# Kernel tuning notes

Hardware: AMD Instinct MI355X
Metric: run time of the kernel (lower is better)

## Reference

```python
import jax, jax.numpy as jnp
import numpy as np
import math

C = 256
K = 64
STAGE_NUM = 3
UNFOLD_SIZES = (1, 3, 5)


def _l2norm(t, axis):
    return t / (1e-6 + jnp.linalg.norm(t, axis=axis, keepdims=True))


def setup_inputs() -> dict:
    key = jax.random.key(0)
    k0, k1, k2 = jax.random.split(key, 3)
    b, h, w = 4, 64, 64
    x = jax.random.normal(k0, (b, C, h, w), dtype=jnp.float32)
    mu0 = jax.random.normal(k1, (1, C, K), dtype=jnp.float32) * math.sqrt(2.0 / K)
    mu0 = _l2norm(mu0, axis=1)  # matches buffer init: normal_(0, sqrt(2/k)) then l2norm over c
    w_scalar = jnp.array(1.0, dtype=jnp.float32)
    # convcat: Conv2d(3c, c, 1); init std = sqrt(2 / (1*1*out_channels)) = sqrt(2/c)
    w_cat = jax.random.normal(k2, (C, 3 * C), dtype=jnp.float32) * math.sqrt(2.0 / C)
    b_cat = jnp.zeros((C,), dtype=jnp.float32)
    return {"x": x, "mu0": mu0, "w": w_scalar, "w_cat": w_cat, "b_cat": b_cat}


def _mwi_forward(x, mu0, w, w_cat, b_cat):
    b, c, h, wd = x.shape
    k = mu0.shape[2]
    mu = jnp.broadcast_to(mu0, (b, c, k))
    feats = []
    for s in UNFOLD_SIZES:
        p = (s - 1) // 2
        xp = jnp.pad(x, ((0, 0), (0, 0), (p, p), (p, p)))
        # im2col: (b, c, s*s, h, w), kernel positions row-major -> matches torch F.unfold then view(b,c,-1)
        patches = jnp.stack([xp[:, :, i:i + h, j:j + wd] for i in range(s) for j in range(s)], axis=2)
        ux = patches.reshape(b, c, s * s * h * wd)  # (b, c, N)
        z = None
        for _ in range(STAGE_NUM):  # EM iterations (no_grad in original)
            z = jax.nn.softmax(jnp.einsum('bcn,bck->bnk', ux, mu), axis=2)  # E-step
            z_ = z / (1e-6 + z.sum(axis=1, keepdims=True))
            mu = _l2norm(jnp.einsum('bcn,bnk->bck', ux, z_), axis=1)  # M-step
        mu = jax.lax.stop_gradient(mu)
        z = jax.lax.stop_gradient(z)
        zf = jnp.einsum('bck,bnk->bcn', mu, z)  # reconstruction (b, c, N)
        zf = zf.reshape(b, c, s, s, h, wd)
        # col2im (F.fold): overlap-add of kernel positions
        out = jnp.zeros((b, c, h + 2 * p, wd + 2 * p), dtype=x.dtype)
        for i in range(s):
            for j in range(s):
                out = out.at[:, :, i:i + h, j:j + wd].add(zf[:, :, i, j])
        feats.append(out[:, :, p:p + h, p:p + wd])
    cat = jnp.concatenate(feats, axis=1)  # (b, 3c, h, w)
    u = jnp.einsum('bihw,oi->bohw', cat, w_cat) + b_cat[None, :, None, None]
    out = jax.nn.relu(u * w + x)
    return out, mu


def reference(x, mu0, w, w_cat, b_cat):
    return _mwi_forward(x, mu0, w, w_cat, b_cat)
```

## Files before the change

kernel.cpp:

```cpp
#include <hip/hip_runtime.h>

typedef float f32x4 __attribute__((ext_vector_type(4)));
typedef short bf16x8 __attribute__((ext_vector_type(8)));
typedef unsigned short u16;
typedef u16 u16x8 __attribute__((ext_vector_type(8)));
typedef unsigned int u32;

#define B 4
#define C 256
#define K 64
#define NN 4096
#define W3C 768
#define CP 264
#define SP 72
#define LGP 68

__device__ __forceinline__ u16 bf_hi(float f) {
    unsigned u = __float_as_uint(f);
    u += 0x7FFFu + ((u >> 16) & 1u);
    return (u16)(u >> 16);
}
__device__ __forceinline__ float bf_f(u16 s) { return __uint_as_float(((unsigned)s) << 16); }

__global__ void k_prep(const float* __restrict__ x, const float* __restrict__ mu0,
                       const float* __restrict__ w_cat,
                       u16* __restrict__ xch, u16* __restrict__ xcl,
                       u16* __restrict__ wch, u16* __restrict__ wcl,
                       u16* __restrict__ muth, u16* __restrict__ mutl,
                       float* __restrict__ tp0) {
    int blk = blockIdx.x, tid = threadIdx.x;
    if (blk < 2048) {
        int i = blk * 256 + tid;
        const float4* s4 = (const float4*)(x + (size_t)i * 8);
        float4 a = s4[0], bq = s4[1];
        float v[8] = {a.x, a.y, a.z, a.w, bq.x, bq.y, bq.z, bq.w};
        u16x8 hv, lv;
        #pragma unroll
        for (int j = 0; j < 8; j++) { u16 hh = bf_hi(v[j]); hv[j] = hh; lv[j] = bf_hi(v[j] - bf_f(hh)); }
        *(u16x8*)(xch + (size_t)i * 8) = hv;
        *(u16x8*)(xcl + (size_t)i * 8) = lv;
    } else if (blk < 2144) {
        int i = (blk - 2048) * 256 + tid;
        const float4* s4 = (const float4*)(w_cat + (size_t)i * 8);
        float4 a = s4[0], bq = s4[1];
        float v[8] = {a.x, a.y, a.z, a.w, bq.x, bq.y, bq.z, bq.w};
        u16x8 hv, lv;
        #pragma unroll
        for (int j = 0; j < 8; j++) { u16 hh = bf_hi(v[j]); hv[j] = hh; lv[j] = bf_hi(v[j] - bf_f(hh)); }
        *(u16x8*)(wch + (size_t)i * 8) = hv;
        *(u16x8*)(wcl + (size_t)i * 8) = lv;
    } else if (blk < 2400) {
        int g = (blk - 2144) * 256 + tid;
        int kq = (g >> 8) & 63, cq = g & 255;
        float v = mu0[cq * K + kq];
        u16 hh = bf_hi(v);
        muth[g] = hh;
        mutl[g] = bf_hi(v - bf_f(hh));
    } else {
        int i = (blk - 2400) * 256 + tid;
        float4 z = {0.f, 0.f, 0.f, 0.f};
        *(float4*)&tp0[(size_t)i * 4] = z;
    }
}

__global__ void k_prept(const float* __restrict__ x, u16* __restrict__ th,
                        u16* __restrict__ tl) {
    __shared__ float tile[32][33];
    int b = blockIdx.z, c0 = blockIdx.y * 32, n0 = blockIdx.x * 32;
    int tx = threadIdx.x, ty = threadIdx.y;
    #pragma unroll
    for (int j = 0; j < 4; j++)
        tile[ty + j * 8][tx] = x[((size_t)(b * C + c0 + ty + j * 8)) * NN + n0 + tx];
    __syncthreads();
    #pragma unroll
    for (int j = 0; j < 4; j++) {
        int n = n0 + ty + j * 8;
        float v = tile[tx][ty + j * 8];
        u16 hh = bf_hi(v);
        size_t o = ((size_t)(b * NN + n)) * C + c0 + tx;
        th[o] = hh;
        tl[o] = bf_hi(v - bf_f(hh));
    }
}

__global__ __launch_bounds__(512) void k_em(
        const u16* __restrict__ xth, const u16* __restrict__ xtl,
        const u16* __restrict__ xch, const u16* __restrict__ xcl,
        const u16* __restrict__ muth, const u16* __restrict__ mutl,
        const float* __restrict__ tp_prev, float* __restrict__ tp_cur,
        float* __restrict__ tp_next, float* __restrict__ dpart,
        u16* __restrict__ sig_out, u16* __restrict__ Pb,
        const u16* __restrict__ wch, const u16* __restrict__ wcl,
        int iter, int pv, float dconst_prev, int write_sig, int s_prev)
{
    extern __shared__ char smem[];
    u16* smh   = (u16*)smem;
    u16* sml   = smh + 64 * CP;
    float* slog = (float*)(sml + 64 * CP);
    u16* sTh   = (u16*)(slog + 64 * LGP);
    u16* sTl   = sTh + 64 * SP;
    float* redf = (float*)(sTl + 64 * SP);

    const int ch = blockIdx.x, b = blockIdx.y, tid = threadIdx.x;
    const int n0 = ch * 64;
    const int w = tid >> 6, l = tid & 63, lg = l >> 4, lr = l & 15;
    f32x4 z4 = {0.f, 0.f, 0.f, 0.f};

    if (tid < 256) tp_next[(size_t)b * K * C + ch * 256 + tid] = 0.f;

    float vals[32];
    float inv = 0.f;
    int kq = tid >> 3, g = tid & 7;
    if (iter == 0) {
        size_t mbase = (size_t)(b * K) * C;
        for (int t = tid; t < 2048; t += 512) {
            int r = t >> 5, cof = (t & 31) * 8;
            *(u16x8*)&smh[r * CP + cof] = *(const u16x8*)&muth[mbase + (size_t)r * C + cof];
            *(u16x8*)&sml[r * CP + cof] = *(const u16x8*)&mutl[mbase + (size_t)r * C + cof];
        }
    } else {
        if (tid < 64) {
            float dv = 0.f;
            #pragma unroll 8
            for (int c2 = 0; c2 < 64; c2++) dv += dpart[((size_t)(b * 64 + c2)) * K + tid];
            redf[1088 + tid] = dv;
        }
        const float* tp = tp_prev + (size_t)b * K * C + (size_t)kq * C + g * 32;
        float ssq = 0.f;
        #pragma unroll
        for (int j4 = 0; j4 < 8; j4++) {
            float4 v4 = *(const float4*)&tp[j4 * 4];
            vals[j4 * 4 + 0] = v4.x; vals[j4 * 4 + 1] = v4.y;
            vals[j4 * 4 + 2] = v4.z; vals[j4 * 4 + 3] = v4.w;
            ssq += v4.x * v4.x + v4.y * v4.y + v4.z * v4.z + v4.w * v4.w;
        }
        #pragma unroll
        for (int off = 1; off <= 4; off <<= 1) ssq += __shfl_xor(ssq, off);
        __syncthreads();
        float d = dconst_prev + redf[1088 + kq];
        inv = 1.f / (1e-6f * d + sqrtf(ssq));
        #pragma unroll
        for (int j8 = 0; j8 < 4; j8++) {
            u16x8 hv, lv;
            #pragma unroll
            for (int j = 0; j < 8; j++) {
                float v = vals[j8 * 8 + j] * inv;
                u16 hh = bf_hi(v);
                hv[j] = hh; lv[j] = bf_hi(v - bf_f(hh));
            }
            *(u16x8*)&smh[kq * CP + g * 32 + j8 * 8] = hv;
            *(u16x8*)&sml[kq * CP + g * 32 + j8 * 8] = lv;
        }
    }
    __syncthreads();

    if (s_prev >= 0 && ch < 4) {
        f32x4 pacc[2] = {z4, z4};
        int orow = ch * 64 + (w & 3) * 16 + lr;
        const u16* wbh = wch + (size_t)orow * W3C + s_prev * C;
        const u16* wbl = wcl + (size_t)orow * W3C + s_prev * C;
        for (int cc = 0; cc < 8; cc++) {
            int co = cc * 32 + lg * 8;
            bf16x8 Ah = *(const bf16x8*)&wbh[co];
            bf16x8 Al = *(const bf16x8*)&wbl[co];
            #pragma unroll
            for (int ktl = 0; ktl < 2; ktl++) {
                int kt = (w >> 2) * 2 + ktl;
                bf16x8 Bh = *(bf16x8*)&smh[(kt * 16 + lr) * CP + co];
                bf16x8 Bl = *(bf16x8*)&sml[(kt * 16 + lr) * CP + co];
                pacc[ktl] = __builtin_amdgcn_mfma_f32_16x16x32_bf16(Ah, Bh, pacc[ktl], 0, 0, 0);
                pacc[ktl] = __builtin_amdgcn_mfma_f32_16x16x32_bf16(Al, Bh, pacc[ktl], 0, 0, 0);
                pacc[ktl] = __builtin_amdgcn_mfma_f32_16x16x32_bf16(Ah, Bl, pacc[ktl], 0, 0, 0);
            }
        }
        #pragma unroll
        for (int ktl = 0; ktl < 2; ktl++)
            #pragma unroll
            for (int jj = 0; jj < 4; jj++) {
                int o = ch * 64 + (w & 3) * 16 + lg * 4 + jj;
                int kk = ((w >> 2) * 2 + ktl) * 16 + lr;
                Pb[((size_t)((s_prev * B + b) * C + o)) * K + kk] = bf_hi(pacc[ktl][jj]);
            }
    }

    f32x4 acc[4] = {z4, z4, z4, z4};
    {
        int chalf = (w >> 2) * 128;
        const u16* xrh = xth + ((size_t)(b * NN + n0 + (w & 3) * 16 + lr)) * C + chalf;
        const u16* xrl = xtl + ((size_t)(b * NN + n0 + (w & 3) * 16 + lr)) * C + chalf;
        for (int cc = 0; cc < 4; cc++) {
            int co = cc * 32 + lg * 8;
            bf16x8 Ah = *(const bf16x8*)&xrh[co];
            bf16x8 Al = *(const bf16x8*)&xrl[co];
            #pragma unroll
            for (int kt = 0; kt < 4; kt++) {
                bf16x8 Bh = *(bf16x8*)&smh[(kt * 16 + lr) * CP + chalf + co];
                bf16x8 Bl = *(bf16x8*)&sml[(kt * 16 + lr) * CP + chalf + co];
                acc[kt] = __builtin_amdgcn_mfma_f32_16x16x32_bf16(Ah, Bh, acc[kt], 0, 0, 0);
                acc[kt] = __builtin_amdgcn_mfma_f32_16x16x32_bf16(Al, Bh, acc[kt], 0, 0, 0);
                acc[kt] = __builtin_amdgcn_mfma_f32_16x16x32_bf16(Ah, Bl, acc[kt], 0, 0, 0);
            }
        }
    }
    if (w < 4) {
        #pragma unroll
        for (int kt = 0; kt < 4; kt++)
            #pragma unroll
            for (int jj = 0; jj < 4; jj++)
                slog[((w & 3) * 16 + lg * 4 + jj) * LGP + kt * 16 + lr] = acc[kt][jj];
    }
    __syncthreads();

    if (w >= 4) {
        float swv[4][4];
        float psum[4] = {0.f, 0.f, 0.f, 0.f};
        #pragma unroll
        for (int jj = 0; jj < 4; jj++) {
            int rloc = (w & 3) * 16 + lg * 4 + jj;
            int n = n0 + rloc;
            float v0 = acc[0][jj] + slog[rloc * LGP + 0 * 16 + lr];
            float v1 = acc[1][jj] + slog[rloc * LGP + 1 * 16 + lr];
            float v2 = acc[2][jj] + slog[rloc * LGP + 2 * 16 + lr];
            float v3 = acc[3][jj] + slog[rloc * LGP + 3 * 16 + lr];
            float m = fmaxf(fmaxf(v0, v1), fmaxf(v2, v3));
            #pragma unroll
            for (int off = 1; off <= 8; off <<= 1) m = fmaxf(m, __shfl_xor(m, off));
            float e0 = __expf(v0 - m), e1 = __expf(v1 - m), e2 = __expf(v2 - m), e3 = __expf(v3 - m);
            float ss = e0 + e1 + e2 + e3;
            #pragma unroll
            for (int off = 1; off <= 8; off <<= 1) ss += __shfl_xor(ss, off);
            int y = n >> 6, xx = n & 63;
            float cnt = (float)((min(pv, y) + min(pv, 63 - y) + 1) * (min(pv, xx) + min(pv, 63 - xx) + 1));
            float sc = cnt / ss;
            swv[jj][0] = e0 * sc; swv[jj][1] = e1 * sc; swv[jj][2] = e2 * sc; swv[jj][3] = e3 * sc;
            #pragma unroll
            for (int kt = 0; kt < 4; kt++) {
                psum[kt] += swv[jj][kt];
                if (write_sig)
                    sig_out[((size_t)(b * NN + n)) * K + kt * 16 + lr] = bf_hi(swv[jj][kt]);
            }
        }
        #pragma unroll
        for (int kt = 0; kt < 4; kt++) {
            #pragma unroll
            for (int jp = 0; jp < 2; jp++) {
                float va = swv[2 * jp][kt], vb = swv[2 * jp + 1][kt];
                u16 ha = bf_hi(va), hb = bf_hi(vb);
                u16 la = bf_hi(va - bf_f(ha)), lb = bf_hi(vb - bf_f(hb));
                int col = (w & 3) * 16 + lg * 4 + 2 * jp;
                *(u32*)&sTh[(kt * 16 + lr) * SP + col] = (u32)ha | ((u32)hb << 16);
                *(u32*)&sTl[(kt * 16 + lr) * SP + col] = (u32)la | ((u32)lb << 16);
            }
            redf[(kt * 16 + lr) * 17 + (w & 3) * 4 + lg] = psum[kt];
        }
    }
    __syncthreads();
    if (tid < 64) {
        float sd = 0.f;
        #pragma unroll
        for (int g2 = 0; g2 < 16; g2++) sd += redf[tid * 17 + g2];
        dpart[((size_t)(b * 64 + ch)) * K + tid] = sd;
    }

    f32x4 macc[8];
    #pragma unroll
    for (int t = 0; t < 8; t++) macc[t] = z4;
    #pragma unroll
    for (int nn2 = 0; nn2 < 2; nn2++) {
        int no = nn2 * 32 + lg * 8;
        bf16x8 Ah[4], Al[4];
        #pragma unroll
        for (int kt2 = 0; kt2 < 4; kt2++) {
            Ah[kt2] = *(bf16x8*)&sTh[(kt2 * 16 + lr) * SP + no];
            Al[kt2] = *(bf16x8*)&sTl[(kt2 * 16 + lr) * SP + no];
        }
        #pragma unroll
        for (int cio = 0; cio < 2; cio++) {
            int c = (w * 2 + cio) * 16 + lr;
            size_t go = ((size_t)(b * C + c)) * NN + n0 + no;
            bf16x8 Bh = *(const bf16x8*)&xch[go];
            bf16x8 Bl = *(const bf16x8*)&xcl[go];
            #pragma unroll
            for (int kt2 = 0; kt2 < 4; kt2++) {
                macc[kt2 * 2 + cio] = __builtin_amdgcn_mfma_f32_16x16x32_bf16(Ah[kt2], Bh, macc[kt2 * 2 + cio], 0, 0, 0);
                macc[kt2 * 2 + cio] = __builtin_amdgcn_mfma_f32_16x16x32_bf16(Al[kt2], Bh, macc[kt2 * 2 + cio], 0, 0, 0);
                macc[kt2 * 2 + cio] = __builtin_amdgcn_mfma_f32_16x16x32_bf16(Ah[kt2], Bl, macc[kt2 * 2 + cio], 0, 0, 0);
            }
        }
    }
    #pragma unroll
    for (int kt2 = 0; kt2 < 4; kt2++)
        #pragma unroll
        for (int cio = 0; cio < 2; cio++)
            #pragma unroll
            for (int jj = 0; jj < 4; jj++) {
                int kk = kt2 * 16 + lg * 4 + jj;
                int c = (w * 2 + cio) * 16 + lr;
                atomicAdd(&tp_cur[((size_t)b * K + kk) * C + c], macc[kt2 * 2 + cio][jj]);
            }
}

__global__ __launch_bounds__(256) void k_pfinal(
        const float* __restrict__ tp_last, const float* __restrict__ dpart,
        const u16* __restrict__ wch, const u16* __restrict__ wcl,
        u16* __restrict__ Pb, float* __restrict__ out_mu, float dconst)
{
    extern __shared__ char smem[];
    u16* smh = (u16*)smem;
    u16* sml = smh + 64 * CP;
    float* redf = (float*)(sml + 64 * CP);
    int ob = blockIdx.x, b = blockIdx.y, tid = threadIdx.x;
    int w = tid >> 6, l = tid & 63, lg = l >> 4, lr = l & 15;
    if (tid < 64) {
        float dv = 0.f;
        #pragma unroll 8
        for (int c2 = 0; c2 < 64; c2++) dv += dpart[((size_t)(b * 64 + c2)) * K + tid];
        redf[tid] = dv;
    }
    __syncthreads();
    {
        int kq = tid >> 2, g = tid & 3;
        const float* tp = tp_last + (size_t)b * K * C + (size_t)kq * C + g * 64;
        float vals[64];
        float ssq = 0.f;
        #pragma unroll
        for (int j4 = 0; j4 < 16; j4++) {
            float4 v4 = *(const float4*)&tp[j4 * 4];
            vals[j4 * 4 + 0] = v4.x; vals[j4 * 4 + 1] = v4.y;
            vals[j4 * 4 + 2] = v4.z; vals[j4 * 4 + 3] = v4.w;
            ssq += v4.x * v4.x + v4.y * v4.y + v4.z * v4.z + v4.w * v4.w;
        }
        ssq += __shfl_xor(ssq, 1);
        ssq += __shfl_xor(ssq, 2);
        float d = dconst + redf[kq];
        float inv = 1.f / (1e-6f * d + sqrtf(ssq));
        #pragma unroll
        for (int j8 = 0; j8 < 8; j8++) {
            u16x8 hv, lv;
            #pragma unroll
            for (int j = 0; j < 8; j++) {
                float v = vals[j8 * 8 + j] * inv;
                u16 hh = bf_hi(v);
                hv[j] = hh; lv[j] = bf_hi(v - bf_f(hh));
            }
            *(u16x8*)&smh[kq * CP + g * 64 + j8 * 8] = hv;
            *(u16x8*)&sml[kq * CP + g * 64 + j8 * 8] = lv;
        }
        if (ob == 0) {
            #pragma unroll 8
            for (int j = 0; j < 64; j++)
                out_mu[((size_t)(b * C + g * 64 + j)) * K + kq] = vals[j] * inv;
        }
    }
    __syncthreads();
    f32x4 pacc[4] = {{0.f,0.f,0.f,0.f},{0.f,0.f,0.f,0.f},{0.f,0.f,0.f,0.f},{0.f,0.f,0.f,0.f}};
    int orow = ob * 64 + w * 16 + lr;
    const u16* wbh = wch + (size_t)orow * W3C + 2 * C;
    const u16* wbl = wcl + (size_t)orow * W3C + 2 * C;
    for (int cc = 0; cc < 8; cc++) {
        int co = cc * 32 + lg * 8;
        bf16x8 Ah = *(const bf16x8*)&wbh[co];
        bf16x8 Al = *(const bf16x8*)&wbl[co];
        #pragma unroll
        for (int kt = 0; kt < 4; kt++) {
            bf16x8 Bh = *(bf16x8*)&smh[(kt * 16 + lr) * CP + co];
            bf16x8 Bl = *(bf16x8*)&sml[(kt * 16 + lr) * CP + co];
            pacc[kt] = __builtin_amdgcn_mfma_f32_16x16x32_bf16(Ah, Bh, pacc[kt], 0, 0, 0);
            pacc[kt] = __builtin_amdgcn_mfma_f32_16x16x32_bf16(Al, Bh, pacc[kt], 0, 0, 0);
            pacc[kt] = __builtin_amdgcn_mfma_f32_16x16x32_bf16(Ah, Bl, pacc[kt], 0, 0, 0);
        }
    }
    #pragma unroll
    for (int kt = 0; kt < 4; kt++)
        #pragma unroll
        for (int jj = 0; jj < 4; jj++) {
            int o = ob * 64 + w * 16 + lg * 4 + jj;
            Pb[((size_t)((2 * B + b) * C + o)) * K + kt * 16 + lr] = bf_hi(pacc[kt][jj]);
        }
}

__global__ __launch_bounds__(256) void k_final(
        const u16* __restrict__ sh_g, const u16* __restrict__ Pb,
        const float* __restrict__ x, const float* __restrict__ b_cat,
        const float* __restrict__ wscal, float* __restrict__ out) {
    __shared__ u16 ssig[64 * 72];
    __shared__ u16 sP[64 * 72];
    __shared__ float tbuf[64 * 68];
    int nt = blockIdx.x, ot = blockIdx.y, b = blockIdx.z;
    int n0 = nt * 64, o0 = ot * 64;
    int tid = threadIdx.x, w = tid >> 6, l = tid & 63, lg = l >> 4, lr = l & 15;
    f32x4 z4 = {0.f, 0.f, 0.f, 0.f};
    f32x4 acc[4] = {z4, z4, z4, z4};
    for (int s = 0; s < 3; s++) {
        __syncthreads();
        for (int t = tid; t < 512; t += 256) {
            int r = t >> 3, kc = (t & 7) * 8;
            *(u16x8*)&ssig[r * 72 + kc] =
                *(const u16x8*)&sh_g[(size_t)s * ((size_t)B * NN * K) + ((size_t)(b * NN + n0 + r)) * K + kc];
            *(u16x8*)&sP[r * 72 + kc] =
                *(const u16x8*)&Pb[((size_t)((s * B + b) * C + o0 + r)) * K + kc];
        }
        __syncthreads();
        #pragma unroll
        for (int kk = 0; kk < 2; kk++) {
            int ko = kk * 32 + lg * 8;
            bf16x8 A = *(bf16x8*)&ssig[(w * 16 + lr) * 72 + ko];
            #pragma unroll
            for (int oi = 0; oi < 4; oi++) {
                bf16x8 Bv = *(bf16x8*)&sP[(oi * 16 + lr) * 72 + ko];
                acc[oi] = __builtin_amdgcn_mfma_f32_16x16x32_bf16(A, Bv, acc[oi], 0, 0, 0);
            }
        }
    }
    __syncthreads();
    #pragma unroll
    for (int oi = 0; oi < 4; oi++)
        #pragma unroll
        for (int jj = 0; jj < 4; jj++)
            tbuf[(oi * 16 + lr) * 68 + (w * 16 + lg * 4 + jj)] = acc[oi][jj];
    __syncthreads();
    float wv = wscal[0];
    for (int t = tid; t < 1024; t += 256) {
        int ol = t >> 4, ck = (t & 15) * 4;
        int o = o0 + ol;
        float bc = b_cat[o];
        float4 u4 = *(float4*)&tbuf[ol * 68 + ck];
        size_t base = ((size_t)(b * C + o)) * NN + n0 + ck;
        float4 xv = *(const float4*)&x[base];
        float4 r;
        r.x = fmaxf((u4.x + bc) * wv + xv.x, 0.f);
        r.y = fmaxf((u4.y + bc) * wv + xv.y, 0.f);
        r.z = fmaxf((u4.z + bc) * wv + xv.z, 0.f);
        r.w = fmaxf((u4.w + bc) * wv + xv.w, 0.f);
        *(float4*)&out[base] = r;
    }
}

extern "C" void kernel_launch(void* const* d_in, const int* in_sizes, int n_in,
                              void* d_out, int out_size, void* d_ws, size_t ws_size,
                              hipStream_t stream) {
    const float* x     = (const float*)d_in[0];
    const float* mu0   = (const float*)d_in[1];
    const float* wsc   = (const float*)d_in[2];
    const float* w_cat = (const float*)d_in[3];
    const float* b_cat = (const float*)d_in[4];
    float* out = (float*)d_out;
    char* wsb = (char*)d_ws;

    const size_t SZ_X2   = (size_t)B * C * NN * 2;
    const size_t SZ_MUT  = (size_t)B * K * C * 2;
    const size_t SZ_SIGH = (size_t)3 * B * NN * K * 2;
    const size_t SZ_TPB  = (size_t)B * K * C * 4;
    const size_t SZ_DP   = (size_t)B * 64 * K * 4;
    const size_t SZ_PB   = (size_t)3 * B * C * K * 2;
    const size_t SZ_WC   = (size_t)C * W3C * 2;

    size_t off = 0;
    u16*   xch  = (u16*)(wsb + off); off += SZ_X2;
    u16*   xcl  = (u16*)(wsb + off); off += SZ_X2;
    u16*   xth  = (u16*)(wsb + off); off += SZ_X2;
    u16*   xtl  = (u16*)(wsb + off); off += SZ_X2;
    u16*   muth = (u16*)(wsb + off); off += SZ_MUT;
    u16*   mutl = (u16*)(wsb + off); off += SZ_MUT;
    u16*   sigh = (u16*)(wsb + off); off += SZ_SIGH;
    float* tpb0 = (float*)(wsb + off); off += SZ_TPB;
    float* tpb1 = (float*)(wsb + off); off += SZ_TPB;
    float* tpb2 = (float*)(wsb + off); off += SZ_TPB;
    float* dpart= (float*)(wsb + off); off += SZ_DP;
    u16*   Pb   = (u16*)(wsb + off); off += SZ_PB;
    u16*   wch  = (u16*)(wsb + off); off += SZ_WC;
    u16*   wcl  = (u16*)(wsb + off); off += SZ_WC;
    float* out_mu = out + (size_t)B * C * NN;
    float* bufs[3] = {tpb0, tpb1, tpb2};

    const int EM_LDS = 2 * 64 * CP * 2 + 64 * LGP * 4 + 2 * 64 * SP * 2 + 1152 * 4;
    const int PF_LDS = 2 * 64 * CP * 2 + 64 * 4;
    hipFuncSetAttribute((const void*)k_em, hipFuncAttributeMaxDynamicSharedMemorySize, EM_LDS);
    hipFuncSetAttribute((const void*)k_pfinal, hipFuncAttributeMaxDynamicSharedMemorySize, PF_LDS);

    k_prep<<<2464, 256, 0, stream>>>(x, mu0, w_cat, xch, xcl, wch, wcl, muth, mutl, tpb0);
    k_prept<<<dim3(128, 8, B), dim3(32, 8), 0, stream>>>(x, xth, xtl);

    const int   pvals[3]   = {0, 1, 2};
    const float dconsts[3] = {1e-6f, 1e-6f + 11.9375f, 1e-6f + 59.4375f};

    for (int i = 0; i < 9; i++) {
        int s = i / 3;
        u16* shs = sigh + (size_t)s * ((size_t)B * NN * K);
        float dprev = (i > 0) ? dconsts[(i - 1) / 3] : 0.f;
        int s_prev = (i > 0 && i % 3 == 0) ? (i / 3 - 1) : -1;
        k_em<<<dim3(64, B), 512, EM_LDS, stream>>>(
            xth, xtl, xch, xcl, muth, mutl,
            bufs[(i + 2) % 3], bufs[i % 3], bufs[(i + 1) % 3], dpart,
            shs, Pb, wch, wcl,
            i, pvals[s], dprev, (i % 3 == 2) ? 1 : 0, s_prev);
    }
    k_pfinal<<<dim3(4, B), 256, PF_LDS, stream>>>(bufs[8 % 3], dpart, wch, wcl,
                                                  Pb, out_mu, dconsts[2]);
    k_final<<<dim3(64, 4, B), 256, 0, stream>>>(sigh, Pb, x, b_cat, wsc, out);
}
```

Measured before the change: 290.7 us.

## Fuse prep, EM iterations and pfinal into one persistent kernel with grid barriers

```diff
diff --git a/kernel.cpp b/kernel.cpp
--- a/kernel.cpp
+++ b/kernel.cpp
@@ -22,123 +22,144 @@
 }
 __device__ __forceinline__ float bf_f(u16 s) { return __uint_as_float(((unsigned)s) << 16); }
 
-__global__ void k_prep(const float* __restrict__ x, const float* __restrict__ mu0,
-                       const float* __restrict__ w_cat,
-                       u16* __restrict__ xch, u16* __restrict__ xcl,
-                       u16* __restrict__ wch, u16* __restrict__ wcl,
-                       u16* __restrict__ muth, u16* __restrict__ mutl,
-                       float* __restrict__ tp0) {
-    int blk = blockIdx.x, tid = threadIdx.x;
-    if (blk < 2048) {
-        int i = blk * 256 + tid;
-        const float4* s4 = (const float4*)(x + (size_t)i * 8);
-        float4 a = s4[0], bq = s4[1];
-        float v[8] = {a.x, a.y, a.z, a.w, bq.x, bq.y, bq.z, bq.w};
-        u16x8 hv, lv;
-        #pragma unroll
-        for (int j = 0; j < 8; j++) { u16 hh = bf_hi(v[j]); hv[j] = hh; lv[j] = bf_hi(v[j] - bf_f(hh)); }
-        *(u16x8*)(xch + (size_t)i * 8) = hv;
-        *(u16x8*)(xcl + (size_t)i * 8) = lv;
-    } else if (blk < 2144) {
-        int i = (blk - 2048) * 256 + tid;
-        const float4* s4 = (const float4*)(w_cat + (size_t)i * 8);
-        float4 a = s4[0], bq = s4[1];
-        float v[8] = {a.x, a.y, a.z, a.w, bq.x, bq.y, bq.z, bq.w};
-        u16x8 hv, lv;
-        #pragma unroll
-        for (int j = 0; j < 8; j++) { u16 hh = bf_hi(v[j]); hv[j] = hh; lv[j] = bf_hi(v[j] - bf_f(hh)); }
-        *(u16x8*)(wch + (size_t)i * 8) = hv;
-        *(u16x8*)(wcl + (size_t)i * 8) = lv;
-    } else if (blk < 2400) {
-        int g = (blk - 2144) * 256 + tid;
-        int kq = (g >> 8) & 63, cq = g & 255;
-        float v = mu0[cq * K + kq];
-        u16 hh = bf_hi(v);
-        muth[g] = hh;
-        mutl[g] = bf_hi(v - bf_f(hh));
-    } else {
-        int i = (blk - 2400) * 256 + tid;
-        float4 z = {0.f, 0.f, 0.f, 0.f};
-        *(float4*)&tp0[(size_t)i * 4] = z;
-    }
+__device__ __forceinline__ void gridbar(u32* cnt, u32 target) {
+    __syncthreads();
+    if (threadIdx.x == 0) {
+        __threadfence();
+        __hip_atomic_fetch_add(cnt, 1u, __ATOMIC_ACQ_REL, __HIP_MEMORY_SCOPE_AGENT);
+        while (__hip_atomic_load(cnt, __ATOMIC_ACQUIRE, __HIP_MEMORY_SCOPE_AGENT) < target)
+            __builtin_amdgcn_s_sleep(2);
+        __threadfence();
+    }
+    __syncthreads();
 }
 
-__global__ void k_prept(const float* __restrict__ x, u16* __restrict__ th,
-                        u16* __restrict__ tl) {
-    __shared__ float tile[32][33];
-    int b = blockIdx.z, c0 = blockIdx.y * 32, n0 = blockIdx.x * 32;
-    int tx = threadIdx.x, ty = threadIdx.y;
-    #pragma unroll
-    for (int j = 0; j < 4; j++)
-        tile[ty + j * 8][tx] = x[((size_t)(b * C + c0 + ty + j * 8)) * NN + n0 + tx];
-    __syncthreads();
-    #pragma unroll
-    for (int j = 0; j < 4; j++) {
-        int n = n0 + ty + j * 8;
-        float v = tile[tx][ty + j * 8];
-        u16 hh = bf_hi(v);
-        size_t o = ((size_t)(b * NN + n)) * C + c0 + tx;
-        th[o] = hh;
-        tl[o] = bf_hi(v - bf_f(hh));
-    }
-}
-
-__global__ __launch_bounds__(512) void k_em(
-        const u16* __restrict__ xth, const u16* __restrict__ xtl,
-        const u16* __restrict__ xch, const u16* __restrict__ xcl,
-        const u16* __restrict__ muth, const u16* __restrict__ mutl,
-        const float* __restrict__ tp_prev, float* __restrict__ tp_cur,
-        float* __restrict__ tp_next, float* __restrict__ dpart,
-        u16* __restrict__ sig_out, u16* __restrict__ Pb,
-        const u16* __restrict__ wch, const u16* __restrict__ wcl,
-        int iter, int pv, float dconst_prev, int write_sig, int s_prev)
+__global__ __launch_bounds__(512, 2) void k_mwi(
+        const float* __restrict__ x, const float* __restrict__ mu0,
+        const float* __restrict__ w_cat,
+        u16* __restrict__ xch, u16* __restrict__ xcl,
+        u16* __restrict__ xth, u16* __restrict__ xtl,
+        u16* __restrict__ sigh,
+        float* __restrict__ tp0, float* __restrict__ tp1, float* __restrict__ tp2,
+        float* __restrict__ dpart, u16* __restrict__ Pb,
+        u16* __restrict__ wch, u16* __restrict__ wcl,
+        float* __restrict__ out_mu, u32* __restrict__ cnt)
 {
     extern __shared__ char smem[];
-    u16* smh   = (u16*)smem;
-    u16* sml   = smh + 64 * CP;
+    u16* smh = (u16*)smem;
+    u16* sml = smh + 64 * CP;
     float* slog = (float*)(sml + 64 * CP);
-    u16* sTh   = (u16*)(slog + 64 * LGP);
-    u16* sTl   = sTh + 64 * SP;
+    u16* sTh = (u16*)(slog + 64 * LGP);
+    u16* sTl = sTh + 64 * SP;
     float* redf = (float*)(sTl + 64 * SP);
+    float* tpose = (float*)smem;
 
     const int ch = blockIdx.x, b = blockIdx.y, tid = threadIdx.x;
+    const int blk = b * 64 + ch;
     const int n0 = ch * 64;
+
+    for (int r = 0; r < 8; r++) {
+        int t = blk * 16 + r * 2 + (tid >> 8);
+        int b2 = t >> 10, rem = t & 1023;
+        int c0 = (rem >> 7) << 5, m0 = (rem & 127) << 5;
+        float* tb = tpose + (tid >> 8) * 1056;
+        int tx = tid & 31, ty = (tid >> 5) & 7;
+        #pragma unroll
+        for (int j = 0; j < 4; j++)
+            tb[(ty + j * 8) * 33 + tx] = x[((size_t)(b2 * C + c0 + ty + j * 8)) * NN + m0 + tx];
+        __syncthreads();
+        #pragma unroll
+        for (int j = 0; j < 4; j++) {
+            float v = tb[tx * 33 + ty + j * 8];
+            u16 hh = bf_hi(v);
+            size_t o = ((size_t)(b2 * NN + m0 + ty + j * 8)) * C + c0 + tx;
+            xth[o] = hh;
+            xtl[o] = bf_hi(v - bf_f(hh));
+        }
+        __syncthreads();
+    }
+    {
+        int gtid = blk * 512 + tid;
+        for (int idx = gtid; idx < 524288 + 24576; idx += 131072) {
+            const float* s8; u16 *dh, *dl; size_t o8;
+            if (idx < 524288) { s8 = x + (size_t)idx * 8; dh = xch; dl = xcl; o8 = (size_t)idx * 8; }
+            else { int j2 = idx - 524288; s8 = w_cat + (size_t)j2 * 8; dh = wch; dl = wcl; o8 = (size_t)j2 * 8; }
+            float4 a = ((const float4*)s8)[0], bq = ((const float4*)s8)[1];
+            float v[8] = {a.x, a.y, a.z, a.w, bq.x, bq.y, bq.z, bq.w};
+            u16x8 hv, lv;
+            #pragma unroll
+            for (int j = 0; j < 8; j++) { u16 hh = bf_hi(v[j]); hv[j] = hh; lv[j] = bf_hi(v[j] - bf_f(hh)); }
+            *(u16x8*)(dh + o8) = hv;
+            *(u16x8*)(dl + o8) = lv;
+        }
+        if (gtid < 65536) tp0[gtid] = 0.f;
+    }
+    gridbar(cnt, 256);
+
     const int w = tid >> 6, l = tid & 63, lg = l >> 4, lr = l & 15;
+    const int chalf = (w >> 2) * 128;
+    bf16x8 eAh[4], eAl[4];
+    {
+        const u16* xrh = xth + ((size_t)(b * NN + n0 + (w & 3) * 16 + lr)) * C + chalf;
+        const u16* xrl = xtl + ((size_t)(b * NN + n0 + (w & 3) * 16 + lr)) * C + chalf;
+        #pragma unroll
+        for (int cc = 0; cc < 4; cc++) {
+            eAh[cc] = *(const bf16x8*)&xrh[cc * 32 + lg * 8];
+            eAl[cc] = *(const bf16x8*)&xrl[cc * 32 + lg * 8];
+        }
+    }
+    bf16x8 mBh[4], mBl[4];
+    #pragma unroll
+    for (int nn2 = 0; nn2 < 2; nn2++)
+        #pragma unroll
+        for (int cio = 0; cio < 2; cio++) {
+            int c = (w * 2 + cio) * 16 + lr;
+            size_t go = ((size_t)(b * C + c)) * NN + n0 + nn2 * 32 + lg * 8;
+            mBh[nn2 * 2 + cio] = *(const bf16x8*)&xch[go];
+            mBl[nn2 * 2 + cio] = *(const bf16x8*)&xcl[go];
+        }
+
     f32x4 z4 = {0.f, 0.f, 0.f, 0.f};
-
-    if (tid < 256) tp_next[(size_t)b * K * C + ch * 256 + tid] = 0.f;
-
-    float vals[32];
-    float inv = 0.f;
-    int kq = tid >> 3, g = tid & 7;
-    if (iter == 0) {
-        size_t mbase = (size_t)(b * K) * C;
-        for (int t = tid; t < 2048; t += 512) {
-            int r = t >> 5, cof = (t & 31) * 8;
-            *(u16x8*)&smh[r * CP + cof] = *(const u16x8*)&muth[mbase + (size_t)r * C + cof];
-            *(u16x8*)&sml[r * CP + cof] = *(const u16x8*)&mutl[mbase + (size_t)r * C + cof];
-        }
-    } else {
-        if (tid < 64) {
-            float dv = 0.f;
-            #pragma unroll 8
-            for (int c2 = 0; c2 < 64; c2++) dv += dpart[((size_t)(b * 64 + c2)) * K + tid];
-            redf[1088 + tid] = dv;
-        }
-        const float* tp = tp_prev + (size_t)b * K * C + (size_t)kq * C + g * 32;
-        float ssq = 0.f;
-        #pragma unroll
-        for (int j4 = 0; j4 < 8; j4++) {
-            float4 v4 = *(const float4*)&tp[j4 * 4];
-            vals[j4 * 4 + 0] = v4.x; vals[j4 * 4 + 1] = v4.y;
-            vals[j4 * 4 + 2] = v4.z; vals[j4 * 4 + 3] = v4.w;
-            ssq += v4.x * v4.x + v4.y * v4.y + v4.z * v4.z + v4.w * v4.w;
-        }
-        #pragma unroll
-        for (int off = 1; off <= 4; off <<= 1) ssq += __shfl_xor(ssq, off);
-        __syncthreads();
-        float d = dconst_prev + redf[1088 + kq];
-        inv = 1.f / (1e-6f * d + sqrtf(ssq));
+    const int kq = tid >> 3, g = tid & 7;
+
+    for (int i = 0; i <= 9; i++) {
+        const bool last = (i == 9);
+        if (last && ch >= 4) return;
+        int ip = i % 3, inx = (i + 1) % 3, ipv = (i + 2) % 3;
+        float* tp_cur  = ip  == 0 ? tp0 : (ip  == 1 ? tp1 : tp2);
+        float* tp_next = inx == 0 ? tp0 : (inx == 1 ? tp1 : tp2);
+        const float* tp_prev = ipv == 0 ? tp0 : (ipv == 1 ? tp1 : tp2);
+
+        float vals[32];
+        float inv;
+        if (i == 0) {
+            #pragma unroll
+            for (int j = 0; j < 32; j++) vals[j] = mu0[(g * 32 + j) * K + kq];
+            inv = 1.f;
+        } else {
+            if (tid < 64) {
+                float dv = 0.f;
+                #pragma unroll 8
+                for (int c2 = 0; c2 < 64; c2++) dv += dpart[((size_t)(b * 64 + c2)) * K + tid];
+                redf[1088 + tid] = dv;
+            }
+            const float* tp = tp_prev + (size_t)b * K * C + (size_t)kq * C + g * 32;
+            float ssq = 0.f;
+            #pragma unroll
+            for (int j4 = 0; j4 < 8; j4++) {
+                float4 v4 = *(const float4*)&tp[j4 * 4];
+                vals[j4 * 4 + 0] = v4.x; vals[j4 * 4 + 1] = v4.y;
+                vals[j4 * 4 + 2] = v4.z; vals[j4 * 4 + 3] = v4.w;
+                ssq += v4.x * v4.x + v4.y * v4.y + v4.z * v4.z + v4.w * v4.w;
+            }
+            #pragma unroll
+            for (int off = 1; off <= 4; off <<= 1) ssq += __shfl_xor(ssq, off);
+            __syncthreads();
+            int si = (i - 1) / 3;
+            float dc = 1e-6f + (si == 0 ? 0.f : (si == 1 ? 11.9375f : 59.4375f));
+            float d = dc + redf[1088 + kq];
+            inv = 1.f / (1e-6f * d + sqrtf(ssq));
+        }
         #pragma unroll
         for (int j8 = 0; j8 < 4; j8++) {
             u16x8 hv, lv;
@@ -151,232 +172,159 @@
             *(u16x8*)&smh[kq * CP + g * 32 + j8 * 8] = hv;
             *(u16x8*)&sml[kq * CP + g * 32 + j8 * 8] = lv;
         }
-    }
-    __syncthreads();
-
-    if (s_prev >= 0 && ch < 4) {
-        f32x4 pacc[2] = {z4, z4};
-        int orow = ch * 64 + (w & 3) * 16 + lr;
-        const u16* wbh = wch + (size_t)orow * W3C + s_prev * C;
-        const u16* wbl = wcl + (size_t)orow * W3C + s_prev * C;
-        for (int cc = 0; cc < 8; cc++) {
-            int co = cc * 32 + lg * 8;
-            bf16x8 Ah = *(const bf16x8*)&wbh[co];
-            bf16x8 Al = *(const bf16x8*)&wbl[co];
-            #pragma unroll
-            for (int ktl = 0; ktl < 2; ktl++) {
-                int kt = (w >> 2) * 2 + ktl;
+        __syncthreads();
+
+        int sp = (i > 0 && i % 3 == 0) ? (i / 3 - 1) : -1;
+        if (sp >= 0 && ch < 4) {
+            f32x4 pacc[2] = {z4, z4};
+            int orow = ch * 64 + (w & 3) * 16 + lr;
+            const u16* wbh = wch + (size_t)orow * W3C + sp * C;
+            const u16* wbl = wcl + (size_t)orow * W3C + sp * C;
+            for (int cc2 = 0; cc2 < 8; cc2++) {
+                int co = cc2 * 32 + lg * 8;
+                bf16x8 Ah = *(const bf16x8*)&wbh[co];
+                bf16x8 Al = *(const bf16x8*)&wbl[co];
+                #pragma unroll
+                for (int ktl = 0; ktl < 2; ktl++) {
+                    int kt = (w >> 2) * 2 + ktl;
+                    bf16x8 Bh = *(bf16x8*)&smh[(kt * 16 + lr) * CP + co];
+                    bf16x8 Bl = *(bf16x8*)&sml[(kt * 16 + lr) * CP + co];
+                    pacc[ktl] = __builtin_amdgcn_mfma_f32_16x16x32_bf16(Ah, Bh, pacc[ktl], 0, 0, 0);
+                    pacc[ktl] = __builtin_amdgcn_mfma_f32_16x16x32_bf16(Al, Bh, pacc[ktl], 0, 0, 0);
+                    pacc[ktl] = __builtin_amdgcn_mfma_f32_16x16x32_bf16(Ah, Bl, pacc[ktl], 0, 0, 0);
+                }
+            }
+            #pragma unroll
+            for (int ktl = 0; ktl < 2; ktl++)
+                #pragma unroll
+                for (int jj = 0; jj < 4; jj++) {
+                    int o = ch * 64 + (w & 3) * 16 + lg * 4 + jj;
+                    int kk = ((w >> 2) * 2 + ktl) * 16 + lr;
+                    Pb[((size_t)((sp * B + b) * C + o)) * K + kk] = bf_hi(pacc[ktl][jj]);
+                }
+        }
+        if (last) {
+            if (ch == 0) {
+                #pragma unroll
+                for (int j = 0; j < 32; j++)
+                    out_mu[((size_t)(b * C + g * 32 + j)) * K + kq] = vals[j] * inv;
+            }
+            return;
+        }
+
+        if (tid < 256) tp_next[(size_t)b * K * C + ch * 256 + tid] = 0.f;
+
+        f32x4 acc[4] = {z4, z4, z4, z4};
+        #pragma unroll
+        for (int cc = 0; cc < 4; cc++) {
+            int co = chalf + cc * 32 + lg * 8;
+            #pragma unroll
+            for (int kt = 0; kt < 4; kt++) {
                 bf16x8 Bh = *(bf16x8*)&smh[(kt * 16 + lr) * CP + co];
                 bf16x8 Bl = *(bf16x8*)&sml[(kt * 16 + lr) * CP + co];
-                pacc[ktl] = __builtin_amdgcn_mfma_f32_16x16x32_bf16(Ah, Bh, pacc[ktl], 0, 0, 0);
-                pacc[ktl] = __builtin_amdgcn_mfma_f32_16x16x32_bf16(Al, Bh, pacc[ktl], 0, 0, 0);
-                pacc[ktl] = __builtin_amdgcn_mfma_f32_16x16x32_bf16(Ah, Bl, pacc[ktl], 0, 0, 0);
-            }
-        }
-        #pragma unroll
-        for (int ktl = 0; ktl < 2; ktl++)
+                acc[kt] = __builtin_amdgcn_mfma_f32_16x16x32_bf16(eAh[cc], Bh, acc[kt], 0, 0, 0);
+                acc[kt] = __builtin_amdgcn_mfma_f32_16x16x32_bf16(eAl[cc], Bh, acc[kt], 0, 0, 0);
+                acc[kt] = __builtin_amdgcn_mfma_f32_16x16x32_bf16(eAh[cc], Bl, acc[kt], 0, 0, 0);
+            }
+        }
+        if (w < 4) {
+            #pragma unroll
+            for (int kt = 0; kt < 4; kt++)
+                #pragma unroll
+                for (int jj = 0; jj < 4; jj++)
+                    slog[((w & 3) * 16 + lg * 4 + jj) * LGP + kt * 16 + lr] = acc[kt][jj];
+        }
+        __syncthreads();
+
+        if (w >= 4) {
+            int pv = i / 3;
+            int write_sig = (i % 3 == 2);
+            u16* sig_out = sigh + (size_t)(i / 3) * ((size_t)B * NN * K);
+            float swv[4][4];
+            float psum[4] = {0.f, 0.f, 0.f, 0.f};
             #pragma unroll
             for (int jj = 0; jj < 4; jj++) {
-                int o = ch * 64 + (w & 3) * 16 + lg * 4 + jj;
-                int kk = ((w >> 2) * 2 + ktl) * 16 + lr;
-                Pb[((size_t)((s_prev * B + b) * C + o)) * K + kk] = bf_hi(pacc[ktl][jj]);
-            }
-    }
-
-    f32x4 acc[4] = {z4, z4, z4, z4};
-    {
-        int chalf = (w >> 2) * 128;
-        const u16* xrh = xth + ((size_t)(b * NN + n0 + (w & 3) * 16 + lr)) * C + chalf;
-        const u16* xrl = xtl + ((size_t)(b * NN + n0 + (w & 3) * 16 + lr)) * C + chalf;
-        for (int cc = 0; cc < 4; cc++) {
-            int co = cc * 32 + lg * 8;
-            bf16x8 Ah = *(const bf16x8*)&xrh[co];
-            bf16x8 Al = *(const bf16x8*)&xrl[co];
+                int rloc = (w & 3) * 16 + lg * 4 + jj;
+                int n = n0 + rloc;
+                float v0 = acc[0][jj] + slog[rloc * LGP + 0 * 16 + lr];
+                float v1 = acc[1][jj] + slog[rloc * LGP + 1 * 16 + lr];
+                float v2 = acc[2][jj] + slog[rloc * LGP + 2 * 16 + lr];
+                float v3 = acc[3][jj] + slog[rloc * LGP + 3 * 16 + lr];
+                float m = fmaxf(fmaxf(v0, v1), fmaxf(v2, v3));
+                #pragma unroll
+                for (int off = 1; off <= 8; off <<= 1) m = fmaxf(m, __shfl_xor(m, off));
+                float e0 = __expf(v0 - m), e1 = __expf(v1 - m), e2 = __expf(v2 - m), e3 = __expf(v3 - m);
+                float ss = e0 + e1 + e2 + e3;
+                #pragma unroll
+                for (int off = 1; off <= 8; off <<= 1) ss += __shfl_xor(ss, off);
+                int y = n >> 6, xx = n & 63;
+                float cntw = (float)((min(pv, y) + min(pv, 63 - y) + 1) * (min(pv, xx) + min(pv, 63 - xx) + 1));
+                float sc = cntw / ss;
+                swv[jj][0] = e0 * sc; swv[jj][1] = e1 * sc; swv[jj][2] = e2 * sc; swv[jj][3] = e3 * sc;
+                #pragma unroll
+                for (int kt = 0; kt < 4; kt++) {
+                    psum[kt] += swv[jj][kt];
+                    if (write_sig)
+                        sig_out[((size_t)(b * NN + n)) * K + kt * 16 + lr] = bf_hi(swv[jj][kt]);
+                }
+            }
             #pragma unroll
             for (int kt = 0; kt < 4; kt++) {
-                bf16x8 Bh = *(bf16x8*)&smh[(kt * 16 + lr) * CP + chalf + co];
-                bf16x8 Bl = *(bf16x8*)&sml[(kt * 16 + lr) * CP + chalf + co];
-                acc[kt] = __builtin_amdgcn_mfma_f32_16x16x32_bf16(Ah, Bh, acc[kt], 0, 0, 0);
-                acc[kt] = __builtin_amdgcn_mfma_f32_16x16x32_bf16(Al, Bh, acc[kt], 0, 0, 0);
-                acc[kt] = __builtin_amdgcn_mfma_f32_16x16x32_bf16(Ah, Bl, acc[kt], 0, 0, 0);
-            }
-        }
-    }
-    if (w < 4) {
-        #pragma unroll
-        for (int kt = 0; kt < 4; kt++)
-            #pragma unroll
-            for (int jj = 0; jj < 4; jj++)
-                slog[((w & 3) * 16 + lg * 4 + jj) * LGP + kt * 16 + lr] = acc[kt][jj];
-    }
-    __syncthreads();
-
-    if (w >= 4) {
-        float swv[4][4];
-        float psum[4] = {0.f, 0.f, 0.f, 0.f};
-        #pragma unroll
-        for (int jj = 0; jj < 4; jj++) {
-            int rloc = (w & 3) * 16 + lg * 4 + jj;
-            int n = n0 + rloc;
-            float v0 = acc[0][jj] + slog[rloc * LGP + 0 * 16 + lr];
-            float v1 = acc[1][jj] + slog[rloc * LGP + 1 * 16 + lr];
-            float v2 = acc[2][jj] + slog[rloc * LGP + 2 * 16 + lr];
-            float v3 = acc[3][jj] + slog[rloc * LGP + 3 * 16 + lr];
-            float m = fmaxf(fmaxf(v0, v1), fmaxf(v2, v3));
-            #pragma unroll
-            for (int off = 1; off <= 8; off <<= 1) m = fmaxf(m, __shfl_xor(m, off));
-            float e0 = __expf(v0 - m), e1 = __expf(v1 - m), e2 = __expf(v2 - m), e3 = __expf(v3 - m);
-            float ss = e0 + e1 + e2 + e3;
-            #pragma unroll
-            for (int off = 1; off <= 8; off <<= 1) ss += __shfl_xor(ss, off);
-            int y = n >> 6, xx = n & 63;
-            float cnt = (float)((min(pv, y) + min(pv, 63 - y) + 1) * (min(pv, xx) + min(pv, 63 - xx) + 1));
-            float sc = cnt / ss;
-            swv[jj][0] = e0 * sc; swv[jj][1] = e1 * sc; swv[jj][2] = e2 * sc; swv[jj][3] = e3 * sc;
-            #pragma unroll
-            for (int kt = 0; kt < 4; kt++) {
-                psum[kt] += swv[jj][kt];
-                if (write_sig)
-                    sig_out[((size_t)(b * NN + n)) * K + kt * 16 + lr] = bf_hi(swv[jj][kt]);
-            }
-        }
-        #pragma unroll
-        for (int kt = 0; kt < 4; kt++) {
-            #pragma unroll
-            for (int jp = 0; jp < 2; jp++) {
-                float va = swv[2 * jp][kt], vb = swv[2 * jp + 1][kt];
-                u16 ha = bf_hi(va), hb = bf_hi(vb);
-                u16 la = bf_hi(va - bf_f(ha)), lb = bf_hi(vb - bf_f(hb));
-                int col = (w & 3) * 16 + lg * 4 + 2 * jp;
-                *(u32*)&sTh[(kt * 16 + lr) * SP + col] = (u32)ha | ((u32)hb << 16);
-                *(u32*)&sTl[(kt * 16 + lr) * SP + col] = (u32)la | ((u32)lb << 16);
-            }
-            redf[(kt * 16 + lr) * 17 + (w & 3) * 4 + lg] = psum[kt];
-        }
-    }
-    __syncthreads();
-    if (tid < 64) {
-        float sd = 0.f;
-        #pragma unroll
-        for (int g2 = 0; g2 < 16; g2++) sd += redf[tid * 17 + g2];
-        dpart[((size_t)(b * 64 + ch)) * K + tid] = sd;
-    }
-
-    f32x4 macc[8];
-    #pragma unroll
-    for (int t = 0; t < 8; t++) macc[t] = z4;
-    #pragma unroll
-    for (int nn2 = 0; nn2 < 2; nn2++) {
-        int no = nn2 * 32 + lg * 8;
-        bf16x8 Ah[4], Al[4];
-        #pragma unroll
-        for (int kt2 = 0; kt2 < 4; kt2++) {
-            Ah[kt2] = *(bf16x8*)&sTh[(kt2 * 16 + lr) * SP + no];
-            Al[kt2] = *(bf16x8*)&sTl[(kt2 * 16 + lr) * SP + no];
-        }
-        #pragma unroll
-        for (int cio = 0; cio < 2; cio++) {
-            int c = (w * 2 + cio) * 16 + lr;
-            size_t go = ((size_t)(b * C + c)) * NN + n0 + no;
-            bf16x8 Bh = *(const bf16x8*)&xch[go];
-            bf16x8 Bl = *(const bf16x8*)&xcl[go];
+                #pragma unroll
+                for (int jp = 0; jp < 2; jp++) {
+                    float va = swv[2 * jp][kt], vb = swv[2 * jp + 1][kt];
+                    u16 ha = bf_hi(va), hb = bf_hi(vb);
+                    u16 la = bf_hi(va - bf_f(ha)), lb = bf_hi(vb - bf_f(hb));
+                    int col = (w & 3) * 16 + lg * 4 + 2 * jp;
+                    *(u32*)&sTh[(kt * 16 + lr) * SP + col] = (u32)ha | ((u32)hb << 16);
+                    *(u32*)&sTl[(kt * 16 + lr) * SP + col] = (u32)la | ((u32)lb << 16);
+                }
+                redf[(kt * 16 + lr) * 17 + (w & 3) * 4 + lg] = psum[kt];
+            }
+        }
+        __syncthreads();
+        if (tid < 64) {
+            float sd = 0.f;
+            #pragma unroll
+            for (int g2 = 0; g2 < 16; g2++) sd += redf[tid * 17 + g2];
+            dpart[((size_t)(b * 64 + ch)) * K + tid] = sd;
+        }
+
+        f32x4 macc[8];
+        #pragma unroll
+        for (int t2 = 0; t2 < 8; t2++) macc[t2] = z4;
+        #pragma unroll
+        for (int nn2 = 0; nn2 < 2; nn2++) {
+            int no = nn2 * 32 + lg * 8;
+            bf16x8 Ah[4], Al[4];
             #pragma unroll
             for (int kt2 = 0; kt2 < 4; kt2++) {
-                macc[kt2 * 2 + cio] = __builtin_amdgcn_mfma_f32_16x16x32_bf16(Ah[kt2], Bh, macc[kt2 * 2 + cio], 0, 0, 0);
-                macc[kt2 * 2 + cio] = __builtin_amdgcn_mfma_f32_16x16x32_bf16(Al[kt2], Bh, macc[kt2 * 2 + cio], 0, 0, 0);
-                macc[kt2 * 2 + cio] = __builtin_amdgcn_mfma_f32_16x16x32_bf16(Ah[kt2], Bl, macc[kt2 * 2 + cio], 0, 0, 0);
-            }
-        }
-    }
-    #pragma unroll
-    for (int kt2 = 0; kt2 < 4; kt2++)
-        #pragma unroll
-        for (int cio = 0; cio < 2; cio++)
-            #pragma unroll
-            for (int jj = 0; jj < 4; jj++) {
-                int kk = kt2 * 16 + lg * 4 + jj;
-                int c = (w * 2 + cio) * 16 + lr;
-                atomicAdd(&tp_cur[((size_t)b * K + kk) * C + c], macc[kt2 * 2 + cio][jj]);
-            }
-}
-
-__global__ __launch_bounds__(256) void k_pfinal(
-        const float* __restrict__ tp_last, const float* __restrict__ dpart,
-        const u16* __restrict__ wch, const u16* __restrict__ wcl,
-        u16* __restrict__ Pb, float* __restrict__ out_mu, float dconst)
-{
-    extern __shared__ char smem[];
-    u16* smh = (u16*)smem;
-    u16* sml = smh + 64 * CP;
-    float* redf = (float*)(sml + 64 * CP);
-    int ob = blockIdx.x, b = blockIdx.y, tid = threadIdx.x;
-    int w = tid >> 6, l = tid & 63, lg = l >> 4, lr = l & 15;
-    if (tid < 64) {
-        float dv = 0.f;
-        #pragma unroll 8
-        for (int c2 = 0; c2 < 64; c2++) dv += dpart[((size_t)(b * 64 + c2)) * K + tid];
-        redf[tid] = dv;
-    }
-    __syncthreads();
-    {
-        int kq = tid >> 2, g = tid & 3;
-        const float* tp = tp_last + (size_t)b * K * C + (size_t)kq * C + g * 64;
-        float vals[64];
-        float ssq = 0.f;
-        #pragma unroll
-        for (int j4 = 0; j4 < 16; j4++) {
-            float4 v4 = *(const float4*)&tp[j4 * 4];
-            vals[j4 * 4 + 0] = v4.x; vals[j4 * 4 + 1] = v4.y;
-            vals[j4 * 4 + 2] = v4.z; vals[j4 * 4 + 3] = v4.w;
-            ssq += v4.x * v4.x + v4.y * v4.y + v4.z * v4.z + v4.w * v4.w;
-        }
-        ssq += __shfl_xor(ssq, 1);
-        ssq += __shfl_xor(ssq, 2);
-        float d = dconst + redf[kq];
-        float inv = 1.f / (1e-6f * d + sqrtf(ssq));
-        #pragma unroll
-        for (int j8 = 0; j8 < 8; j8++) {
-            u16x8 hv, lv;
-            #pragma unroll
-            for (int j = 0; j < 8; j++) {
-                float v = vals[j8 * 8 + j] * inv;
-                u16 hh = bf_hi(v);
-                hv[j] = hh; lv[j] = bf_hi(v - bf_f(hh));
-            }
-            *(u16x8*)&smh[kq * CP + g * 64 + j8 * 8] = hv;
-            *(u16x8*)&sml[kq * CP + g * 64 + j8 * 8] = lv;
-        }
-        if (ob == 0) {
-            #pragma unroll 8
-            for (int j = 0; j < 64; j++)
-                out_mu[((size_t)(b * C + g * 64 + j)) * K + kq] = vals[j] * inv;
-        }
-    }
-    __syncthreads();
-    f32x4 pacc[4] = {{0.f,0.f,0.f,0.f},{0.f,0.f,0.f,0.f},{0.f,0.f,0.f,0.f},{0.f,0.f,0.f,0.f}};
-    int orow = ob * 64 + w * 16 + lr;
-    const u16* wbh = wch + (size_t)orow * W3C + 2 * C;
-    const u16* wbl = wcl + (size_t)orow * W3C + 2 * C;
-    for (int cc = 0; cc < 8; cc++) {
-        int co = cc * 32 + lg * 8;
-        bf16x8 Ah = *(const bf16x8*)&wbh[co];
-        bf16x8 Al = *(const bf16x8*)&wbl[co];
-        #pragma unroll
-        for (int kt = 0; kt < 4; kt++) {
-            bf16x8 Bh = *(bf16x8*)&smh[(kt * 16 + lr) * CP + co];
-            bf16x8 Bl = *(bf16x8*)&sml[(kt * 16 + lr) * CP + co];
-            pacc[kt] = __builtin_amdgcn_mfma_f32_16x16x32_bf16(Ah, Bh, pacc[kt], 0, 0, 0);
-            pacc[kt] = __builtin_amdgcn_mfma_f32_16x16x32_bf16(Al, Bh, pacc[kt], 0, 0, 0);
-            pacc[kt] = __builtin_amdgcn_mfma_f32_16x16x32_bf16(Ah, Bl, pacc[kt], 0, 0, 0);
-        }
-    }
-    #pragma unroll
-    for (int kt = 0; kt < 4; kt++)
-        #pragma unroll
-        for (int jj = 0; jj < 4; jj++) {
-            int o = ob * 64 + w * 16 + lg * 4 + jj;
-            Pb[((size_t)((2 * B + b) * C + o)) * K + kt * 16 + lr] = bf_hi(pacc[kt][jj]);
-        }
+                Ah[kt2] = *(bf16x8*)&sTh[(kt2 * 16 + lr) * SP + no];
+                Al[kt2] = *(bf16x8*)&sTl[(kt2 * 16 + lr) * SP + no];
+            }
+            #pragma unroll
+            for (int cio = 0; cio < 2; cio++) {
+                #pragma unroll
+                for (int kt2 = 0; kt2 < 4; kt2++) {
+                    macc[kt2 * 2 + cio] = __builtin_amdgcn_mfma_f32_16x16x32_bf16(Ah[kt2], mBh[nn2 * 2 + cio], macc[kt2 * 2 + cio], 0, 0, 0);
+                    macc[kt2 * 2 + cio] = __builtin_amdgcn_mfma_f32_16x16x32_bf16(Al[kt2], mBh[nn2 * 2 + cio], macc[kt2 * 2 + cio], 0, 0, 0);
+                    macc[kt2 * 2 + cio] = __builtin_amdgcn_mfma_f32_16x16x32_bf16(Ah[kt2], mBl[nn2 * 2 + cio], macc[kt2 * 2 + cio], 0, 0, 0);
+                }
+            }
+        }
+        #pragma unroll
+        for (int kt2 = 0; kt2 < 4; kt2++)
+            #pragma unroll
+            for (int cio = 0; cio < 2; cio++)
+                #pragma unroll
+                for (int jj = 0; jj < 4; jj++) {
+                    int kk = kt2 * 16 + lg * 4 + jj;
+                    int c = (w * 2 + cio) * 16 + lr;
+                    atomicAdd(&tp_cur[((size_t)b * K + kk) * C + c], macc[kt2 * 2 + cio][jj]);
+                }
+
+        gridbar(cnt, (u32)(i + 2) * 256);
+    }
 }
 
 __global__ __launch_bounds__(256) void k_final(
@@ -448,7 +396,6 @@
     char* wsb = (char*)d_ws;
 
     const size_t SZ_X2   = (size_t)B * C * NN * 2;
-    const size_t SZ_MUT  = (size_t)B * K * C * 2;
     const size_t SZ_SIGH = (size_t)3 * B * NN * K * 2;
     const size_t SZ_TPB  = (size_t)B * K * C * 4;
     const size_t SZ_DP   = (size_t)B * 64 * K * 4;
@@ -460,42 +407,23 @@
     u16*   xcl  = (u16*)(wsb + off); off += SZ_X2;
     u16*   xth  = (u16*)(wsb + off); off += SZ_X2;
     u16*   xtl  = (u16*)(wsb + off); off += SZ_X2;
-    u16*   muth = (u16*)(wsb + off); off += SZ_MUT;
-    u16*   mutl = (u16*)(wsb + off); off += SZ_MUT;
     u16*   sigh = (u16*)(wsb + off); off += SZ_SIGH;
-    float* tpb0 = (float*)(wsb + off); off += SZ_TPB;
-    float* tpb1 = (float*)(wsb + off); off += SZ_TPB;
-    float* tpb2 = (float*)(wsb + off); off += SZ_TPB;
+    float* tp0  = (float*)(wsb + off); off += SZ_TPB;
+    float* tp1  = (float*)(wsb + off); off += SZ_TPB;
+    float* tp2  = (float*)(wsb + off); off += SZ_TPB;
     float* dpart= (float*)(wsb + off); off += SZ_DP;
     u16*   Pb   = (u16*)(wsb + off); off += SZ_PB;
     u16*   wch  = (u16*)(wsb + off); off += SZ_WC;
     u16*   wcl  = (u16*)(wsb + off); off += SZ_WC;
+    u32*   cnt  = (u32*)(wsb + off); off += 256;
     float* out_mu = out + (size_t)B * C * NN;
-    float* bufs[3] = {tpb0, tpb1, tpb2};
-
-    const int EM_LDS = 2 * 64 * CP * 2 + 64 * LGP * 4 + 2 * 64 * SP * 2 + 1152 * 4;
-    const int PF_LDS = 2 * 64 * CP * 2 + 64 * 4;
-    hipFuncSetAttribute((const void*)k_em, hipFuncAttributeMaxDynamicSharedMemorySize, EM_LDS);
-    hipFuncSetAttribute((const void*)k_pfinal, hipFuncAttributeMaxDynamicSharedMemorySize, PF_LDS);
-
-    k_prep<<<2464, 256, 0, stream>>>(x, mu0, w_cat, xch, xcl, wch, wcl, muth, mutl, tpb0);
-    k_prept<<<dim3(128, 8, B), dim3(32, 8), 0, stream>>>(x, xth, xtl);
-
-    const int   pvals[3]   = {0, 1, 2};
-    const float dconsts[3] = {1e-6f, 1e-6f + 11.9375f, 1e-6f + 59.4375f};
-
-    for (int i = 0; i < 9; i++) {
-        int s = i / 3;
-        u16* shs = sigh + (size_t)s * ((size_t)B * NN * K);
-        float dprev = (i > 0) ? dconsts[(i - 1) / 3] : 0.f;
-        int s_prev = (i > 0 && i % 3 == 0) ? (i / 3 - 1) : -1;
-        k_em<<<dim3(64, B), 512, EM_LDS, stream>>>(
-            xth, xtl, xch, xcl, muth, mutl,
-            bufs[(i + 2) % 3], bufs[i % 3], bufs[(i + 1) % 3], dpart,
-            shs, Pb, wch, wcl,
-            i, pvals[s], dprev, (i % 3 == 2) ? 1 : 0, s_prev);
-    }
-    k_pfinal<<<dim3(4, B), 256, PF_LDS, stream>>>(bufs[8 % 3], dpart, wch, wcl,
-                                                  Pb, out_mu, dconsts[2]);
+
+    const int MWI_LDS = 2 * 64 * CP * 2 + 64 * LGP * 4 + 2 * 64 * SP * 2 + 1152 * 4;
+    hipFuncSetAttribute((const void*)k_mwi, hipFuncAttributeMaxDynamicSharedMemorySize, MWI_LDS);
+
+    hipMemsetAsync(cnt, 0, sizeof(u32), stream);
+    k_mwi<<<dim3(64, B), 512, MWI_LDS, stream>>>(
+        x, mu0, w_cat, xch, xcl, xth, xtl, sigh,
+        tp0, tp1, tp2, dpart, Pb, wch, wcl, out_mu, cnt);
     k_final<<<dim3(64, 4, B), 256, 0, stream>>>(sigh, Pb, x, b_cat, wsc, out);
 }
```

After: 656.1 us. 126% more time.
